# Performance work log

Hardware: AMD Instinct MI355X
Metric: run time of the kernel (lower is better)

## Reference

```python
import jax, jax.numpy as jnp
import numpy as np

S, B, D_IN, D_SRC, D_ALIGN = 2048, 64, 512, 512, 512


def setup_inputs() -> dict:
    key = jax.random.key(0)
    ks = jax.random.split(key, 6)
    scale = 0.1  # matches uniform_(-0.1, 0.1) init magnitude
    return {
        "input": jax.random.normal(ks[0], (1, B, D_IN), dtype=jnp.float32),
        "source_hids": jax.random.normal(ks[1], (S, B, D_SRC), dtype=jnp.float32),
        "encoder_padding_mask": jnp.zeros((S, B), dtype=bool),
        "W1": jax.random.uniform(ks[2], (D_ALIGN, D_IN + D_SRC), jnp.float32, -scale, scale),
        "b1": jax.random.uniform(ks[3], (D_ALIGN,), jnp.float32, -scale, scale),
        "W2": jax.random.uniform(ks[4], (1, D_ALIGN), jnp.float32, -scale, scale),
        "b2": jax.random.uniform(ks[5], (1,), jnp.float32, -scale, scale),
    }


def reference(input, source_hids, encoder_padding_mask, W1, b1, W2, b2):
    # input: [1, B, D_in] broadcast over srclen; source_hids: [S, B, D_src]
    s = source_hids.shape[0]
    x = jnp.broadcast_to(input, (s,) + input.shape[1:])          # [S, B, D_in]
    cat = jnp.concatenate((x, source_hids), axis=-1)             # [S, B, D_in+D_src]
    h = jnp.tanh(jnp.einsum('sbd,ad->sba', cat, W1) + b1)        # [S, B, D_align]
    scores = jnp.einsum('sba,oa->sbo', h, W2)[..., 0] + b2[0]    # [S, B]
    scores = jnp.where(encoder_padding_mask, -jnp.inf, scores)
    attn = jax.nn.softmax(scores, axis=0)                        # softmax over srclen
    ctx = jnp.einsum('sb,sbd->bd', attn, source_hids)            # [B, D_src]
    return ctx, attn
```

## Files before the change

### kernel.cpp

```cpp
#include <hip/hip_runtime.h>
#include <hip/hip_bf16.h>
#include <math.h>

#define S_LEN 2048
#define BATCH 64
#define DDIM 512

typedef __attribute__((ext_vector_type(8))) short bf16x8;
typedef __attribute__((ext_vector_type(4))) float f32x4;
typedef __attribute__((ext_vector_type(4))) unsigned int u32x4;

typedef __attribute__((address_space(1))) const void g_void;
typedef __attribute__((address_space(3))) void l_void;

#define ROT8(n) ((((n) ^ ((n) >> 3))) & 7)

__device__ __forceinline__ unsigned short f2bf(float f) {
  unsigned int u = __float_as_uint(f);
  u += 0x7fffu + ((u >> 16) & 1u);
  return (unsigned short)(u >> 16);
}

__device__ __forceinline__ float tanh_fast(float x) {
  float e = __builtin_amdgcn_exp2f(x * 2.88539008177793f);
  return 1.0f - 2.0f * __builtin_amdgcn_rcpf(e + 1.0f);
}

__global__ __launch_bounds__(256) void prep_kernel(
    const float* __restrict__ W1, const float* __restrict__ b1,
    const float* __restrict__ input, unsigned short* __restrict__ W1b,
    float* __restrict__ uprime) {
  __shared__ float w1row[1024];
  const int a = blockIdx.x;
  const int t = threadIdx.x;
  float4 v = *(const float4*)(W1 + a * 1024 + t * 4);
  *(float4*)(w1row + t * 4) = v;
  if (t >= 128) {
    ushort4 u;
    u.x = f2bf(v.x); u.y = f2bf(v.y); u.z = f2bf(v.z); u.w = f2bf(v.w);
    *(ushort4*)(W1b + a * 512 + (t * 4 - 512)) = u;
  }
  __syncthreads();
  if (t < BATCH) {
    const float4* inp = (const float4*)(input + t * 512);
    const float4* wr = (const float4*)w1row;
    float acc = b1[a];
#pragma unroll 4
    for (int d = 0; d < 128; ++d) {
      float4 x = inp[d], w = wr[d];
      acc += x.x * w.x + x.y * w.y + x.z * w.z + x.w * w.w;
    }
    uprime[t * 512 + a] = acc;
  }
}

#define ASTR 72

__global__ __launch_bounds__(256, 3) void scores_kernel(
    const float* __restrict__ src, const unsigned short* __restrict__ W1b,
    const float* __restrict__ uprime, const float* __restrict__ W2,
    float* __restrict__ scores_g) {
  __shared__ unsigned short A_sm[128 * ASTR];
  __shared__ unsigned short B_sm[128 * 64];
  __shared__ float s_lds[128];

  const int t = threadIdx.x;
  const int m0 = blockIdx.x >> 2;
  const int n0 = (blockIdx.x & 3) << 7;
  const int w = t >> 6;
  const int lane = t & 63;
  const int quad = lane >> 4;
  const int l15 = lane & 15;
  const int mw = w & 1, nw = w >> 1;

  if (t < 128) s_lds[t] = 0.f;

  f32x4 acc[4][4];
#pragma unroll
  for (int i = 0; i < 4; ++i)
#pragma unroll
    for (int j = 0; j < 4; ++j) acc[i][j] = (f32x4){0.f, 0.f, 0.f, 0.f};

  const int arow = t >> 1;
  const int ahalf = t & 1;
  const float* gA = src + (size_t)(m0 * 128 + arow) * DDIM + ahalf * 32;
  unsigned short* ldsA = A_sm + arow * ASTR + ahalf * 32;

  const int brow = lane >> 3;
  const int bchunk = lane & 7;
  const unsigned short* gB[4];
  unsigned short* ldsB[4];
#pragma unroll
  for (int g = 0; g < 4; ++g) {
    const int nl = w * 32 + g * 8 + brow;
    gB[g] = W1b + (size_t)(n0 + nl) * DDIM + ((bchunk ^ ROT8(nl)) << 3);
    ldsB[g] = B_sm + (w * 32 + g * 8) * 64;
  }

  for (int k0 = 0; k0 < DDIM; k0 += 64) {
#pragma unroll
    for (int g = 0; g < 4; ++g)
      __builtin_amdgcn_global_load_lds((g_void*)gB[g], (l_void*)ldsB[g], 16, 0, 0);
    float4 v[8];
#pragma unroll
    for (int f = 0; f < 8; ++f) v[f] = ((const float4*)gA)[f];
#pragma unroll
    for (int f = 0; f < 4; ++f) {
      unsigned x0 = __float_as_uint(v[2 * f].x) + 0x8000u;
      unsigned y0 = __float_as_uint(v[2 * f].y) + 0x8000u;
      unsigned z0 = __float_as_uint(v[2 * f].z) + 0x8000u;
      unsigned w0 = __float_as_uint(v[2 * f].w) + 0x8000u;
      unsigned x1 = __float_as_uint(v[2 * f + 1].x) + 0x8000u;
      unsigned y1 = __float_as_uint(v[2 * f + 1].y) + 0x8000u;
      unsigned z1 = __float_as_uint(v[2 * f + 1].z) + 0x8000u;
      unsigned w1 = __float_as_uint(v[2 * f + 1].w) + 0x8000u;
      u32x4 o;
      o.x = __builtin_amdgcn_perm(y0, x0, 0x07060302u);
      o.y = __builtin_amdgcn_perm(w0, z0, 0x07060302u);
      o.z = __builtin_amdgcn_perm(y1, x1, 0x07060302u);
      o.w = __builtin_amdgcn_perm(w1, z1, 0x07060302u);
      *(u32x4*)(ldsA + f * 8) = o;
    }
    gA += 64;
#pragma unroll
    for (int g = 0; g < 4; ++g) gB[g] += 64;
    __syncthreads();

#pragma unroll
    for (int ks = 0; ks < 2; ++ks) {
      bf16x8 af[4], bfr[4];
#pragma unroll
      for (int i = 0; i < 4; ++i)
        af[i] = *(const bf16x8*)(A_sm + (mw * 64 + i * 16 + l15) * ASTR + ks * 32 + quad * 8);
#pragma unroll
      for (int j = 0; j < 4; ++j) {
        const int nl = nw * 64 + j * 16 + l15;
        af[0] = af[0];
        bfr[j] = *(const bf16x8*)(B_sm + nl * 64 + (((ks * 4 + quad) ^ ROT8(nl)) << 3));
      }
#pragma unroll
      for (int i = 0; i < 4; ++i)
#pragma unroll
        for (int j = 0; j < 4; ++j)
          acc[i][j] = __builtin_amdgcn_mfma_f32_16x16x32_bf16(af[i], bfr[j], acc[i][j], 0, 0, 0);
    }
    __syncthreads();
  }

  float w2r[4];
#pragma unroll
  for (int j = 0; j < 4; ++j) w2r[j] = W2[n0 + nw * 64 + j * 16 + l15];

#pragma unroll
  for (int i = 0; i < 4; ++i) {
#pragma unroll
    for (int r = 0; r < 4; ++r) {
      const int rloc = mw * 64 + i * 16 + quad * 4 + r;
      const int b = rloc & 63;
      const float* up = uprime + b * 512 + n0 + nw * 64 + l15;
      float sp = 0.f;
#pragma unroll
      for (int j = 0; j < 4; ++j)
        sp += w2r[j] * tanh_fast(acc[i][j][r] + up[j * 16]);
      sp += __shfl_xor(sp, 1);
      sp += __shfl_xor(sp, 2);
      sp += __shfl_xor(sp, 4);
      sp += __shfl_xor(sp, 8);
      if (l15 == 0) atomicAdd(&s_lds[rloc], sp);
    }
  }
  __syncthreads();
  if (t < 128) atomicAdd(scores_g + m0 * 128 + t, s_lds[t]);
}

__global__ __launch_bounds__(256) void softmax_kernel(
    const float* __restrict__ scores_g, const unsigned char* __restrict__ mask,
    float* __restrict__ attn_g) {
  __shared__ float red[256];
  const int b = blockIdx.x, t = threadIdx.x;
  float m = -__builtin_inff();
  float sc[8];
#pragma unroll
  for (int c = 0; c < 8; ++c) {
    const int s = t + c * 256;
    sc[c] = mask[s * BATCH + b] ? -__builtin_inff() : scores_g[s * BATCH + b];
    m = fmaxf(m, sc[c]);
  }
  red[t] = m;
  __syncthreads();
  for (int off = 128; off; off >>= 1) {
    if (t < off) red[t] = fmaxf(red[t], red[t + off]);
    __syncthreads();
  }
  m = red[0];
  __syncthreads();
  float sum = 0.f;
#pragma unroll
  for (int c = 0; c < 8; ++c) sum += __expf(sc[c] - m);
  red[t] = sum;
  __syncthreads();
  for (int off = 128; off; off >>= 1) {
    if (t < off) red[t] += red[t + off];
    __syncthreads();
  }
  const float inv = 1.f / red[0];
#pragma unroll
  for (int c = 0; c < 8; ++c)
    attn_g[(t + c * 256) * BATCH + b] = __expf(sc[c] - m) * inv;
}

__global__ __launch_bounds__(256) void ctx_kernel(
    const float* __restrict__ src, const float* __restrict__ attn_g,
    float* __restrict__ ctx) {
  __shared__ float a_lds[128];
  const int s0 = blockIdx.x * 128, b = blockIdx.y, t = threadIdx.x;
  if (t < 128) a_lds[t] = attn_g[(s0 + t) * BATCH + b];
  __syncthreads();
  const int f4i = t & 127;
  const int sh = t >> 7;
  const float4* base = (const float4*)src + ((size_t)(s0 + sh * 64) * BATCH + b) * 128 + f4i;
  float4 acc = {0.f, 0.f, 0.f, 0.f};
#pragma unroll 8
  for (int i = 0; i < 64; ++i) {
    const float a = a_lds[sh * 64 + i];
    float4 v = base[(size_t)i * BATCH * 128];
    acc.x += a * v.x; acc.y += a * v.y; acc.z += a * v.z; acc.w += a * v.w;
  }
  float* cp = ctx + b * DDIM + f4i * 4;
  atomicAdd(cp + 0, acc.x);
  atomicAdd(cp + 1, acc.y);
  atomicAdd(cp + 2, acc.z);
  atomicAdd(cp + 3, acc.w);
}

extern "C" void kernel_launch(void* const* d_in, const int* in_sizes, int n_in,
                              void* d_out, int out_size, void* d_ws, size_t ws_size,
                              hipStream_t stream) {
  const float* input = (const float*)d_in[0];
  const float* src = (const float*)d_in[1];
  const unsigned char* mask = (const unsigned char*)d_in[2];
  const float* W1 = (const float*)d_in[3];
  const float* b1 = (const float*)d_in[4];
  const float* W2 = (const float*)d_in[5];

  float* ctx = (float*)d_out;
  float* attn = (float*)d_out + BATCH * DDIM;

  unsigned short* W1b = (unsigned short*)d_ws;
  float* uprime = (float*)((char*)d_ws + 512 * 1024);
  float* scores = (float*)((char*)d_ws + 512 * 1024 + 128 * 1024);

  hipMemsetAsync(ctx, 0, BATCH * DDIM * sizeof(float), stream);
  hipMemsetAsync(scores, 0, S_LEN * BATCH * sizeof(float), stream);
  prep_kernel<<<512, 256, 0, stream>>>(W1, b1, input, W1b, uprime);
  scores_kernel<<<4096, 256, 0, stream>>>(src, W1b, uprime, W2, scores);
  softmax_kernel<<<BATCH, 256, 0, stream>>>(scores, mask, attn);
  ctx_kernel<<<dim3(16, BATCH), 256, 0, stream>>>(src, attn, ctx);
}
```

Measured before the change: 577.0 us.

## Retile scores GEMM per source position with full-N tiles and atomic-free ctx reduction

The scores kernel now gives each block one source position (64 batch rows) and all 512 alignment columns, using 8 waves. The whole B tile lives in LDS and the result is written straight into transposed scores, so the global atomics and the scores memset are gone. The ctx computation becomes a partial-sum kernel plus a reduce kernel, replacing float atomics and the ctx memset, with a fallback when the workspace is too small. The cost is a much larger LDS footprint, 64KB for B per block, and W1b being re-streamed from cache by every block.

```diff
diff --git a/kernel.cpp b/kernel.cpp
--- a/kernel.cpp
+++ b/kernel.cpp
@@ -12,8 +12,6 @@
 
 typedef __attribute__((address_space(1))) const void g_void;
 typedef __attribute__((address_space(3))) void l_void;
-
-#define ROT8(n) ((((n) ^ ((n) >> 3))) & 7)
 
 __device__ __forceinline__ unsigned short f2bf(float f) {
   unsigned int u = __float_as_uint(f);
@@ -54,26 +52,22 @@
   }
 }
 
-#define ASTR 72
-
-__global__ __launch_bounds__(256, 3) void scores_kernel(
+__global__ __launch_bounds__(512, 4) void scores_kernel(
     const float* __restrict__ src, const unsigned short* __restrict__ W1b,
     const float* __restrict__ uprime, const float* __restrict__ W2,
-    float* __restrict__ scores_g) {
-  __shared__ unsigned short A_sm[128 * ASTR];
-  __shared__ unsigned short B_sm[128 * 64];
-  __shared__ float s_lds[128];
+    float* __restrict__ scores_t) {
+  __shared__ unsigned short A_sm[64 * 64];
+  __shared__ unsigned short B_sm[512 * 64];
+  __shared__ float s_lds[BATCH];
 
   const int t = threadIdx.x;
-  const int m0 = blockIdx.x >> 2;
-  const int n0 = (blockIdx.x & 3) << 7;
+  const int s = blockIdx.x;
   const int w = t >> 6;
   const int lane = t & 63;
   const int quad = lane >> 4;
   const int l15 = lane & 15;
-  const int mw = w & 1, nw = w >> 1;
-
-  if (t < 128) s_lds[t] = 0.f;
+
+  if (t < BATCH) s_lds[t] = 0.f;
 
   f32x4 acc[4][4];
 #pragma unroll
@@ -81,62 +75,53 @@
 #pragma unroll
     for (int j = 0; j < 4; ++j) acc[i][j] = (f32x4){0.f, 0.f, 0.f, 0.f};
 
-  const int arow = t >> 1;
-  const int ahalf = t & 1;
-  const float* gA = src + (size_t)(m0 * 128 + arow) * DDIM + ahalf * 32;
-  unsigned short* ldsA = A_sm + arow * ASTR + ahalf * 32;
-
-  const int brow = lane >> 3;
-  const int bchunk = lane & 7;
-  const unsigned short* gB[4];
-  unsigned short* ldsB[4];
-#pragma unroll
-  for (int g = 0; g < 4; ++g) {
-    const int nl = w * 32 + g * 8 + brow;
-    gB[g] = W1b + (size_t)(n0 + nl) * DDIM + ((bchunk ^ ROT8(nl)) << 3);
-    ldsB[g] = B_sm + (w * 32 + g * 8) * 64;
-  }
+  const float* srcblk = src + (size_t)s * (BATCH * DDIM);
+  const int ar = t >> 3, ap = t & 7, ac = ap ^ (ar & 7);
+  const float* gA = srcblk + ar * DDIM + ac * 8;
+  unsigned short* ldsA = A_sm + ar * 64 + ap * 8;
+  const int br = lane >> 3, bp = lane & 7, bc = bp ^ (br & 7);
+  const unsigned short* gBl = W1b + br * DDIM + bc * 8;
 
   for (int k0 = 0; k0 < DDIM; k0 += 64) {
 #pragma unroll
-    for (int g = 0; g < 4; ++g)
-      __builtin_amdgcn_global_load_lds((g_void*)gB[g], (l_void*)ldsB[g], 16, 0, 0);
-    float4 v[8];
-#pragma unroll
-    for (int f = 0; f < 8; ++f) v[f] = ((const float4*)gA)[f];
-#pragma unroll
-    for (int f = 0; f < 4; ++f) {
-      unsigned x0 = __float_as_uint(v[2 * f].x) + 0x8000u;
-      unsigned y0 = __float_as_uint(v[2 * f].y) + 0x8000u;
-      unsigned z0 = __float_as_uint(v[2 * f].z) + 0x8000u;
-      unsigned w0 = __float_as_uint(v[2 * f].w) + 0x8000u;
-      unsigned x1 = __float_as_uint(v[2 * f + 1].x) + 0x8000u;
-      unsigned y1 = __float_as_uint(v[2 * f + 1].y) + 0x8000u;
-      unsigned z1 = __float_as_uint(v[2 * f + 1].z) + 0x8000u;
-      unsigned w1 = __float_as_uint(v[2 * f + 1].w) + 0x8000u;
+    for (int g = 0; g < 8; ++g) {
+      const unsigned short* gp = gBl + (g * 64 + w * 8) * DDIM + k0;
+      unsigned short* lp = B_sm + (g * 64 + w * 8) * 64;
+      __builtin_amdgcn_global_load_lds((g_void*)gp, (l_void*)lp, 16, 0, 0);
+    }
+    {
+      const float4 v0 = *(const float4*)(gA + k0);
+      const float4 v1 = *(const float4*)(gA + k0 + 4);
+      unsigned x0 = __float_as_uint(v0.x) + 0x8000u;
+      unsigned y0 = __float_as_uint(v0.y) + 0x8000u;
+      unsigned z0 = __float_as_uint(v0.z) + 0x8000u;
+      unsigned w0 = __float_as_uint(v0.w) + 0x8000u;
+      unsigned x1 = __float_as_uint(v1.x) + 0x8000u;
+      unsigned y1 = __float_as_uint(v1.y) + 0x8000u;
+      unsigned z1 = __float_as_uint(v1.z) + 0x8000u;
+      unsigned w1 = __float_as_uint(v1.w) + 0x8000u;
       u32x4 o;
       o.x = __builtin_amdgcn_perm(y0, x0, 0x07060302u);
       o.y = __builtin_amdgcn_perm(w0, z0, 0x07060302u);
       o.z = __builtin_amdgcn_perm(y1, x1, 0x07060302u);
       o.w = __builtin_amdgcn_perm(w1, z1, 0x07060302u);
-      *(u32x4*)(ldsA + f * 8) = o;
-    }
-    gA += 64;
-#pragma unroll
-    for (int g = 0; g < 4; ++g) gB[g] += 64;
+      *(u32x4*)ldsA = o;
+    }
     __syncthreads();
 
 #pragma unroll
     for (int ks = 0; ks < 2; ++ks) {
+      const int c = ks * 4 + quad;
       bf16x8 af[4], bfr[4];
 #pragma unroll
-      for (int i = 0; i < 4; ++i)
-        af[i] = *(const bf16x8*)(A_sm + (mw * 64 + i * 16 + l15) * ASTR + ks * 32 + quad * 8);
+      for (int i = 0; i < 4; ++i) {
+        const int r = i * 16 + l15;
+        af[i] = *(const bf16x8*)(A_sm + r * 64 + ((c ^ (r & 7)) << 3));
+      }
 #pragma unroll
       for (int j = 0; j < 4; ++j) {
-        const int nl = nw * 64 + j * 16 + l15;
-        af[0] = af[0];
-        bfr[j] = *(const bf16x8*)(B_sm + nl * 64 + (((ks * 4 + quad) ^ ROT8(nl)) << 3));
+        const int n = w * 64 + j * 16 + l15;
+        bfr[j] = *(const bf16x8*)(B_sm + n * 64 + ((c ^ (n & 7)) << 3));
       }
 #pragma unroll
       for (int i = 0; i < 4; ++i)
@@ -149,15 +134,14 @@
 
   float w2r[4];
 #pragma unroll
-  for (int j = 0; j < 4; ++j) w2r[j] = W2[n0 + nw * 64 + j * 16 + l15];
+  for (int j = 0; j < 4; ++j) w2r[j] = W2[w * 64 + j * 16 + l15];
 
 #pragma unroll
   for (int i = 0; i < 4; ++i) {
 #pragma unroll
     for (int r = 0; r < 4; ++r) {
-      const int rloc = mw * 64 + i * 16 + quad * 4 + r;
-      const int b = rloc & 63;
-      const float* up = uprime + b * 512 + n0 + nw * 64 + l15;
+      const int b = i * 16 + quad * 4 + r;
+      const float* up = uprime + b * 512 + w * 64 + l15;
       float sp = 0.f;
 #pragma unroll
       for (int j = 0; j < 4; ++j)
@@ -166,16 +150,16 @@
       sp += __shfl_xor(sp, 2);
       sp += __shfl_xor(sp, 4);
       sp += __shfl_xor(sp, 8);
-      if (l15 == 0) atomicAdd(&s_lds[rloc], sp);
-    }
-  }
-  __syncthreads();
-  if (t < 128) atomicAdd(scores_g + m0 * 128 + t, s_lds[t]);
+      if (l15 == 0) atomicAdd(&s_lds[b], sp);
+    }
+  }
+  __syncthreads();
+  if (t < BATCH) scores_t[t * S_LEN + s] = s_lds[t];
 }
 
 __global__ __launch_bounds__(256) void softmax_kernel(
-    const float* __restrict__ scores_g, const unsigned char* __restrict__ mask,
-    float* __restrict__ attn_g) {
+    const float* __restrict__ scores_t, const unsigned char* __restrict__ mask,
+    float* __restrict__ attn_g, float* __restrict__ attn_t, int write_t) {
   __shared__ float red[256];
   const int b = blockIdx.x, t = threadIdx.x;
   float m = -__builtin_inff();
@@ -183,7 +167,7 @@
 #pragma unroll
   for (int c = 0; c < 8; ++c) {
     const int s = t + c * 256;
-    sc[c] = mask[s * BATCH + b] ? -__builtin_inff() : scores_g[s * BATCH + b];
+    sc[c] = mask[s * BATCH + b] ? -__builtin_inff() : scores_t[b * S_LEN + s];
     m = fmaxf(m, sc[c]);
   }
   red[t] = m;
@@ -205,11 +189,51 @@
   }
   const float inv = 1.f / red[0];
 #pragma unroll
-  for (int c = 0; c < 8; ++c)
-    attn_g[(t + c * 256) * BATCH + b] = __expf(sc[c] - m) * inv;
-}
-
-__global__ __launch_bounds__(256) void ctx_kernel(
+  for (int c = 0; c < 8; ++c) {
+    const int s = t + c * 256;
+    const float p = __expf(sc[c] - m) * inv;
+    attn_g[s * BATCH + b] = p;
+    if (write_t) attn_t[b * S_LEN + s] = p;
+  }
+}
+
+__global__ __launch_bounds__(256) void ctx_partial_kernel(
+    const float* __restrict__ src, const float* __restrict__ attn_t,
+    float* __restrict__ partial) {
+  __shared__ float a_lds[64];
+  const int c = blockIdx.x;
+  const int b = blockIdx.y;
+  const int t = threadIdx.x;
+  if (t < 64) a_lds[t] = attn_t[b * S_LEN + c * 64 + t];
+  __syncthreads();
+  const int f4i = t & 127;
+  const int sh = t >> 7;
+  const float4* base =
+      (const float4*)src + ((size_t)(c * 64 + sh * 32) * BATCH + b) * 128 + f4i;
+  float4 acc = {0.f, 0.f, 0.f, 0.f};
+#pragma unroll 8
+  for (int i = 0; i < 32; ++i) {
+    const float a = a_lds[sh * 32 + i];
+    float4 v = base[(size_t)i * BATCH * 128];
+    acc.x += a * v.x; acc.y += a * v.y; acc.z += a * v.z; acc.w += a * v.w;
+  }
+  ((float4*)partial)[((size_t)(c * 2 + sh) * BATCH + b) * 128 + f4i] = acc;
+}
+
+__global__ __launch_bounds__(256) void ctx_reduce_kernel(
+    const float* __restrict__ partial, float* __restrict__ ctx) {
+  const int b = blockIdx.x, t = threadIdx.x;
+  const float2* p = (const float2*)partial + (size_t)b * 256 + t;
+  float2 acc = {0.f, 0.f};
+#pragma unroll 8
+  for (int c2 = 0; c2 < 64; ++c2) {
+    float2 v = p[(size_t)c2 * BATCH * 256];
+    acc.x += v.x; acc.y += v.y;
+  }
+  ((float2*)ctx)[b * 256 + t] = acc;
+}
+
+__global__ __launch_bounds__(256) void ctx_atomic_kernel(
     const float* __restrict__ src, const float* __restrict__ attn_g,
     float* __restrict__ ctx) {
   __shared__ float a_lds[128];
@@ -218,7 +242,8 @@
   __syncthreads();
   const int f4i = t & 127;
   const int sh = t >> 7;
-  const float4* base = (const float4*)src + ((size_t)(s0 + sh * 64) * BATCH + b) * 128 + f4i;
+  const float4* base =
+      (const float4*)src + ((size_t)(s0 + sh * 64) * BATCH + b) * 128 + f4i;
   float4 acc = {0.f, 0.f, 0.f, 0.f};
 #pragma unroll 8
   for (int i = 0; i < 64; ++i) {
@@ -248,12 +273,23 @@
 
   unsigned short* W1b = (unsigned short*)d_ws;
   float* uprime = (float*)((char*)d_ws + 512 * 1024);
-  float* scores = (float*)((char*)d_ws + 512 * 1024 + 128 * 1024);
-
-  hipMemsetAsync(ctx, 0, BATCH * DDIM * sizeof(float), stream);
-  hipMemsetAsync(scores, 0, S_LEN * BATCH * sizeof(float), stream);
+  float* scores_t = (float*)((char*)d_ws + 640 * 1024);
+  float* attn_t = (float*)((char*)d_ws + 1152 * 1024);
+  float* partial = (float*)((char*)d_ws + 1664 * 1024);
+  const size_t NEED_ATTN_T = 1664 * 1024;
+  const size_t NEED_PARTIAL = 1664 * 1024 + (size_t)64 * BATCH * DDIM * 4;
+  const int have_attn_t = ws_size >= NEED_ATTN_T;
+  const int have_partial = ws_size >= NEED_PARTIAL;
+
   prep_kernel<<<512, 256, 0, stream>>>(W1, b1, input, W1b, uprime);
-  scores_kernel<<<4096, 256, 0, stream>>>(src, W1b, uprime, W2, scores);
-  softmax_kernel<<<BATCH, 256, 0, stream>>>(scores, mask, attn);
-  ctx_kernel<<<dim3(16, BATCH), 256, 0, stream>>>(src, attn, ctx);
-}
+  scores_kernel<<<S_LEN, 512, 0, stream>>>(src, W1b, uprime, W2, scores_t);
+  softmax_kernel<<<BATCH, 256, 0, stream>>>(scores_t, mask, attn, attn_t,
+                                            have_attn_t && have_partial);
+  if (have_partial) {
+    ctx_partial_kernel<<<dim3(32, BATCH), 256, 0, stream>>>(src, attn_t, partial);
+    ctx_reduce_kernel<<<BATCH, 256, 0, stream>>>(partial, ctx);
+  } else {
+    hipMemsetAsync(ctx, 0, BATCH * DDIM * sizeof(float), stream);
+    ctx_atomic_kernel<<<dim3(16, BATCH), 256, 0, stream>>>(src, attn, ctx);
+  }
+}
```

Measured after the change: 493.8 us. 14.4% less time.
